# Kernel optimization log

Measured on AMD Instinct MI355X. Metric: run time of the kernel, lower is better.

Reference implementation:

```python
import jax, jax.numpy as jnp
import numpy as np

D_MODEL = 1024
N_HEADS = 16
D_HEAD = D_MODEL // N_HEADS


def setup_inputs() -> dict:
    key = jax.random.key(0)
    ks = jax.random.split(key, 7)
    x = jax.random.normal(ks[0], (1, 4096, D_MODEL), dtype=jnp.float32)
    # torch Linear default init ~ U(-1/sqrt(fan_in), 1/sqrt(fan_in)); small randn is fine for a reference
    Wqkv = jax.random.normal(ks[1], (3 * D_MODEL, D_MODEL), dtype=jnp.float32) * (1.0 / np.sqrt(D_MODEL))
    bqkv = jax.random.normal(ks[2], (3 * D_MODEL,), dtype=jnp.float32) * 0.01
    Wo = jax.random.normal(ks[3], (D_MODEL, D_MODEL), dtype=jnp.float32) * (1.0 / np.sqrt(D_MODEL))
    bo = jax.random.normal(ks[4], (D_MODEL,), dtype=jnp.float32) * 0.01
    wq = jnp.ones((D_HEAD,), dtype=jnp.float32)
    wk = jnp.ones((D_HEAD,), dtype=jnp.float32)
    return {"x": x, "Wqkv": Wqkv, "bqkv": bqkv, "Wo": Wo, "bo": bo, "wq": wq, "wk": wk}


def _rmsnorm(x, w):
    # matches RMSNormRef: mean of squares over last dim, eps added to mean before sqrt
    xf = x.astype(jnp.float32)
    rms = jnp.mean(xf * xf, axis=-1, keepdims=True)
    return (xf / jnp.sqrt(rms + 1e-6) * w.astype(jnp.float32)).astype(x.dtype)


def reference(x, Wqkv, bqkv, Wo, bo, wq, wk):
    b, s, d = x.shape
    qkv = x @ Wqkv.T + bqkv                       # [b, s, 3d]
    q, k, v = jnp.split(qkv, 3, axis=-1)
    q = q.reshape(b, s, N_HEADS, D_HEAD)
    k = k.reshape(b, s, N_HEADS, D_HEAD)
    v = v.reshape(b, s, N_HEADS, D_HEAD)
    q = _rmsnorm(q, wq)
    k = _rmsnorm(k, wk)
    # NOTE: original applies NO 1/sqrt(d_head) scaling and NO causal mask
    qf = q.astype(jnp.float32)
    kf = k.astype(jnp.float32)
    vf = v.astype(jnp.float32)
    attn = jnp.einsum('bqhd,bkhd->bhqk', qf, kf)  # [b, h, s, s] fp32 scores
    attn = jax.nn.softmax(attn, axis=-1)
    z = jnp.einsum('bhqk,bkhd->bqhd', attn, vf).astype(x.dtype)
    z = z.reshape(b, s, d)
    return z @ Wo.T + bo
```

## Files before the change

### kernel.cpp

```cpp
#include <hip/hip_runtime.h>
#include <hip/hip_bf16.h>

typedef __bf16 bf16;
typedef bf16 bf16x8 __attribute__((ext_vector_type(8)));
typedef bf16 bf16x4 __attribute__((ext_vector_type(4)));
typedef float f32x4 __attribute__((ext_vector_type(4)));

static constexpr int SEQ    = 4096;
static constexpr int DMODEL = 1024;
static constexpr int NHEADS = 16;
static constexpr int DHEAD  = 64;
static constexpr int QKV3   = 3 * DMODEL;
static constexpr float SMAX = 64.0f;

__device__ inline void gld16(const bf16* g, bf16* l) {
    __builtin_amdgcn_global_load_lds(
        (const __attribute__((address_space(1))) void*)g,
        (__attribute__((address_space(3))) void*)l, 16, 0, 0);
}

__device__ inline bf16x8 load8(const float* src) {
    float4 a = *(const float4*)(src);
    float4 b = *(const float4*)(src + 4);
    bf16x8 r;
    r[0] = (bf16)a.x; r[1] = (bf16)a.y; r[2] = (bf16)a.z; r[3] = (bf16)a.w;
    r[4] = (bf16)b.x; r[5] = (bf16)b.y; r[6] = (bf16)b.z; r[7] = (bf16)b.w;
    return r;
}

static constexpr size_t NX = (size_t)SEQ * DMODEL;
static constexpr size_t NW = (size_t)QKV3 * DMODEL;
static constexpr size_t NO = (size_t)DMODEL * DMODEL;

__global__ __launch_bounds__(256)
void cvt_all(const float* __restrict__ x, const float* __restrict__ Wqkv,
             const float* __restrict__ Wo, bf16* __restrict__ outbase) {
    const size_t e = ((size_t)blockIdx.x * 256 + threadIdx.x) * 8;
    const float* src;
    if (e < NX)            src = x + e;
    else if (e < NX + NW)  src = Wqkv + (e - NX);
    else                   src = Wo + (e - NX - NW);
    *(bf16x8*)(outbase + e) = load8(src);
}

__global__ __launch_bounds__(256)
void gemm_qkv(const bf16* __restrict__ A, const bf16* __restrict__ W,
              const float* __restrict__ bias, const float* __restrict__ wq,
              const float* __restrict__ wk, bf16* __restrict__ qkv,
              bf16* __restrict__ Vt) {
    __shared__ __align__(16) bf16 As[128 * 32];
    __shared__ __align__(16) bf16 Ws[128 * 32];
    const int tid  = threadIdx.x;
    const int wave = tid >> 6;
    const int ll   = tid & 15;
    const int quad = (tid & 63) >> 4;
    const int wm   = (wave >> 1) * 64;
    const int wn   = (wave & 1) * 64;
    const int m0 = blockIdx.y * 128;
    const int n0 = blockIdx.x * 128;

    f32x4 acc[4][4];
#pragma unroll
    for (int i = 0; i < 4; ++i)
#pragma unroll
        for (int j = 0; j < 4; ++j) acc[i][j] = (f32x4){0.f, 0.f, 0.f, 0.f};

    for (int k0 = 0; k0 < DMODEL; k0 += 32) {
        __syncthreads();
#pragma unroll
        for (int i = 0; i < 2; ++i) {
            const int idx = i * 256 + tid;
            const int row = idx >> 2;
            const int c   = (idx & 3) ^ ((row >> 1) & 3);
            gld16(&A[(size_t)(m0 + row) * DMODEL + k0 + c * 8], As + idx * 8);
            gld16(&W[(size_t)(n0 + row) * DMODEL + k0 + c * 8], Ws + idx * 8);
        }
        __syncthreads();
        bf16x8 af[4], bfr[4];
#pragma unroll
        for (int mi = 0; mi < 4; ++mi) {
            const int row = wm + mi * 16 + ll;
            af[mi] = *(const bf16x8*)(As + (row * 4 + (quad ^ ((ll >> 1) & 3))) * 8);
        }
#pragma unroll
        for (int ni = 0; ni < 4; ++ni) {
            const int row = wn + ni * 16 + ll;
            bfr[ni] = *(const bf16x8*)(Ws + (row * 4 + (quad ^ ((ll >> 1) & 3))) * 8);
        }
#pragma unroll
        for (int mi = 0; mi < 4; ++mi)
#pragma unroll
            for (int ni = 0; ni < 4; ++ni)
                acc[mi][ni] = __builtin_amdgcn_mfma_f32_16x16x32_bf16(
                    af[mi], bfr[ni], acc[mi][ni], 0, 0, 0);
    }

    float bvn[4];
#pragma unroll
    for (int ni = 0; ni < 4; ++ni) bvn[ni] = bias[n0 + wn + ni * 16 + ll];

    const int sect = (n0 + wn) >> 10;
    if (sect < 2) {
        const float* wv = sect ? wk : wq;
        float wvl[4];
#pragma unroll
        for (int ni = 0; ni < 4; ++ni) wvl[ni] = wv[ni * 16 + ll];
#pragma unroll
        for (int mi = 0; mi < 4; ++mi)
#pragma unroll
            for (int r = 0; r < 4; ++r) {
                float xf[4];
                float ss = 0.f;
#pragma unroll
                for (int ni = 0; ni < 4; ++ni) {
                    xf[ni] = (float)(bf16)(acc[mi][ni][r] + bvn[ni]);
                    ss += xf[ni] * xf[ni];
                }
#pragma unroll
                for (int off = 1; off < 16; off <<= 1) ss += __shfl_xor(ss, off);
                const float scale = rsqrtf(ss * (1.0f / 64.0f) + 1e-6f);
                const int row = m0 + wm + mi * 16 + quad * 4 + r;
#pragma unroll
                for (int ni = 0; ni < 4; ++ni)
                    qkv[(size_t)row * QKV3 + n0 + wn + ni * 16 + ll] =
                        (bf16)(xf[ni] * scale * wvl[ni]);
            }
    } else {
        const int h = (n0 + wn - 2 * DMODEL) >> 6;
#pragma unroll
        for (int mi = 0; mi < 4; ++mi) {
            const int kv = m0 + wm + mi * 16 + quad * 4;
#pragma unroll
            for (int ni = 0; ni < 4; ++ni) {
                bf16x4 vv;
#pragma unroll
                for (int r = 0; r < 4; ++r) vv[r] = (bf16)(acc[mi][ni][r] + bvn[ni]);
                *(bf16x4*)(Vt + (size_t)(h * DHEAD + ni * 16 + ll) * SEQ + kv) = vv;
            }
        }
    }
}

__global__ __launch_bounds__(256)
void gemm_out(const bf16* __restrict__ A, const bf16* __restrict__ W,
              const float* __restrict__ bias, float* __restrict__ C) {
    __shared__ __align__(16) bf16 As[128 * 32];
    __shared__ __align__(16) bf16 Ws[64 * 32];
    const int tid  = threadIdx.x;
    const int wave = tid >> 6;
    const int ll   = tid & 15;
    const int quad = (tid & 63) >> 4;
    const int m0 = blockIdx.y * 128;
    const int n0 = blockIdx.x * 64;

    f32x4 acc[2][4];
#pragma unroll
    for (int i = 0; i < 2; ++i)
#pragma unroll
        for (int j = 0; j < 4; ++j) acc[i][j] = (f32x4){0.f, 0.f, 0.f, 0.f};

    for (int k0 = 0; k0 < DMODEL; k0 += 32) {
        __syncthreads();
#pragma unroll
        for (int i = 0; i < 2; ++i) {
            const int idx = i * 256 + tid;
            const int row = idx >> 2;
            const int c   = (idx & 3) ^ ((row >> 1) & 3);
            gld16(&A[(size_t)(m0 + row) * DMODEL + k0 + c * 8], As + idx * 8);
        }
        {
            const int j   = tid;
            const int row = j >> 2;
            const int c   = (j & 3) ^ ((row >> 1) & 3);
            gld16(&W[(size_t)(n0 + row) * DMODEL + k0 + c * 8], Ws + j * 8);
        }
        __syncthreads();
        bf16x8 af[2], bfr[4];
#pragma unroll
        for (int mi = 0; mi < 2; ++mi) {
            const int row = wave * 32 + mi * 16 + ll;
            af[mi] = *(const bf16x8*)(As + (row * 4 + (quad ^ ((ll >> 1) & 3))) * 8);
        }
#pragma unroll
        for (int ni = 0; ni < 4; ++ni) {
            const int row = ni * 16 + ll;
            bfr[ni] = *(const bf16x8*)(Ws + (row * 4 + (quad ^ ((ll >> 1) & 3))) * 8);
        }
#pragma unroll
        for (int mi = 0; mi < 2; ++mi)
#pragma unroll
            for (int ni = 0; ni < 4; ++ni)
                acc[mi][ni] = __builtin_amdgcn_mfma_f32_16x16x32_bf16(
                    af[mi], bfr[ni], acc[mi][ni], 0, 0, 0);
    }
#pragma unroll
    for (int ni = 0; ni < 4; ++ni) {
        const int col = n0 + ni * 16 + ll;
        const float bv = bias[col];
#pragma unroll
        for (int mi = 0; mi < 2; ++mi)
#pragma unroll
            for (int r = 0; r < 4; ++r) {
                const int row = m0 + wave * 32 + mi * 16 + quad * 4 + r;
                C[(size_t)row * DMODEL + col] = acc[mi][ni][r] + bv;
            }
    }
}

template<bool PARTIAL>
__global__ __launch_bounds__(256, 4)
void attn_fwd(const bf16* __restrict__ qkv, const bf16* __restrict__ Vt,
              bf16* __restrict__ z, float* __restrict__ opf,
              float* __restrict__ lsum) {
    __shared__ __align__(16) bf16 Ks[64 * 64];
    __shared__ __align__(16) bf16 VTs[64 * 64];
    __shared__ __align__(16) bf16 Ps[128 * 72];

    const int tid  = threadIdx.x;
    const int wave = tid >> 6;
    const int ll   = tid & 15;
    const int quad = (tid & 63) >> 4;
    const int head = blockIdx.x;
    const int q0   = blockIdx.y * 128;
    const int half = PARTIAL ? blockIdx.z : 0;
    const int kvbeg = half * (SEQ / 2);
    const int kvlen = PARTIAL ? (SEQ / 2) : SEQ;
    const int wrow = wave * 32;

    const bf16* kbase  = qkv + DMODEL + head * DHEAD;
    const bf16* vtbase = Vt + (size_t)head * DHEAD * SEQ;

#pragma unroll
    for (int i = 0; i < 4; ++i) {
        const int idx = i * 256 + tid;
        const int row = idx >> 3;
        const int c   = (idx & 7) ^ (row & 7);
        gld16(qkv + (size_t)(q0 + row) * QKV3 + head * DHEAD + c * 8, Ps + idx * 8);
    }
    __syncthreads();
    bf16x8 aq[2][2];
#pragma unroll
    for (int sub = 0; sub < 2; ++sub)
#pragma unroll
        for (int ks = 0; ks < 2; ++ks) {
            const int row = wrow + sub * 16 + ll;
            const int pc  = (ks * 4 + quad) ^ (ll & 7);
            aq[sub][ks] = *(const bf16x8*)(Ps + (row * 8 + pc) * 8);
        }

    f32x4 lp[2];
    f32x4 o[2][4];
#pragma unroll
    for (int sub = 0; sub < 2; ++sub) {
        lp[sub] = (f32x4){0.f, 0.f, 0.f, 0.f};
#pragma unroll
        for (int nt = 0; nt < 4; ++nt) o[sub][nt] = (f32x4){0.f, 0.f, 0.f, 0.f};
    }

    for (int kv0 = kvbeg; kv0 < kvbeg + kvlen; kv0 += 64) {
        __syncthreads();
#pragma unroll
        for (int i = 0; i < 2; ++i) {
            const int idx = i * 256 + tid;
            const int row = idx >> 3;
            const int c   = (idx & 7) ^ (row & 7);
            gld16(kbase + (size_t)(kv0 + row) * QKV3 + c * 8, Ks + idx * 8);
            gld16(vtbase + (size_t)row * SEQ + kv0 + c * 8, VTs + idx * 8);
        }
        __syncthreads();

        f32x4 s[2][4];
#pragma unroll
        for (int nt = 0; nt < 4; ++nt) {
            s[0][nt] = (f32x4){0.f, 0.f, 0.f, 0.f};
            s[1][nt] = (f32x4){0.f, 0.f, 0.f, 0.f};
        }
#pragma unroll
        for (int ks = 0; ks < 2; ++ks)
#pragma unroll
            for (int nt = 0; nt < 4; ++nt) {
                const int row = nt * 16 + ll;
                const int pc  = (ks * 4 + quad) ^ (ll & 7);
                bf16x8 b = *(const bf16x8*)(Ks + (row * 8 + pc) * 8);
                s[0][nt] = __builtin_amdgcn_mfma_f32_16x16x32_bf16(aq[0][ks], b, s[0][nt], 0, 0, 0);
                s[1][nt] = __builtin_amdgcn_mfma_f32_16x16x32_bf16(aq[1][ks], b, s[1][nt], 0, 0, 0);
            }

#pragma unroll
        for (int sub = 0; sub < 2; ++sub) {
#pragma unroll
            for (int nt = 0; nt < 4; ++nt)
#pragma unroll
                for (int r = 0; r < 4; ++r) {
                    const float p2 = __expf(s[sub][nt][r] - SMAX);
                    s[sub][nt][r] = p2;
                    lp[sub][r] += p2;
                }
#pragma unroll
            for (int nt = 0; nt < 4; ++nt)
#pragma unroll
                for (int r = 0; r < 4; ++r)
                    Ps[(wrow + sub * 16 + quad * 4 + r) * 72 + nt * 16 + ll] =
                        (bf16)s[sub][nt][r];
        }

#pragma unroll
        for (int ks = 0; ks < 2; ++ks) {
            bf16x8 a0 = *(const bf16x8*)(Ps + (wrow + ll) * 72 + ks * 32 + quad * 8);
            bf16x8 a1 = *(const bf16x8*)(Ps + (wrow + 16 + ll) * 72 + ks * 32 + quad * 8);
#pragma unroll
            for (int nt = 0; nt < 4; ++nt) {
                const int row = nt * 16 + ll;
                const int pc  = (ks * 4 + quad) ^ (ll & 7);
                bf16x8 b = *(const bf16x8*)(VTs + (row * 8 + pc) * 8);
                o[0][nt] = __builtin_amdgcn_mfma_f32_16x16x32_bf16(a0, b, o[0][nt], 0, 0, 0);
                o[1][nt] = __builtin_amdgcn_mfma_f32_16x16x32_bf16(a1, b, o[1][nt], 0, 0, 0);
            }
        }
    }

#pragma unroll
    for (int sub = 0; sub < 2; ++sub) {
#pragma unroll
        for (int off = 1; off < 16; off <<= 1)
#pragma unroll
            for (int r = 0; r < 4; ++r) lp[sub][r] += __shfl_xor(lp[sub][r], off);

        if (PARTIAL) {
#pragma unroll
            for (int nt = 0; nt < 4; ++nt) {
                const int col = head * DHEAD + nt * 16 + ll;
#pragma unroll
                for (int r = 0; r < 4; ++r) {
                    const int row = q0 + wrow + sub * 16 + quad * 4 + r;
                    opf[((size_t)half * SEQ + row) * DMODEL + col] = o[sub][nt][r];
                }
            }
            if (ll == 0) {
#pragma unroll
                for (int r = 0; r < 4; ++r) {
                    const int row = q0 + wrow + sub * 16 + quad * 4 + r;
                    lsum[((size_t)half * SEQ + row) * NHEADS + head] = lp[sub][r];
                }
            }
        } else {
#pragma unroll
            for (int nt = 0; nt < 4; ++nt) {
                const int d = head * DHEAD + nt * 16 + ll;
#pragma unroll
                for (int r = 0; r < 4; ++r) {
                    const int row = q0 + wrow + sub * 16 + quad * 4 + r;
                    z[(size_t)row * DMODEL + d] = (bf16)(o[sub][nt][r] / lp[sub][r]);
                }
            }
        }
    }
}

__global__ __launch_bounds__(256)
void combine_halves(const float* __restrict__ opf, const float* __restrict__ lsum,
                    bf16* __restrict__ z) {
    const int row = blockIdx.x;
    const int c   = threadIdx.x * 4;
    const int head = c >> 6;
    const float l = lsum[(size_t)row * NHEADS + head] +
                    lsum[((size_t)SEQ + row) * NHEADS + head];
    const float4 o0 = *(const float4*)(opf + (size_t)row * DMODEL + c);
    const float4 o1 = *(const float4*)(opf + ((size_t)SEQ + row) * DMODEL + c);
    bf16x4 out;
    out[0] = (bf16)((o0.x + o1.x) / l);
    out[1] = (bf16)((o0.y + o1.y) / l);
    out[2] = (bf16)((o0.z + o1.z) / l);
    out[3] = (bf16)((o0.w + o1.w) / l);
    *(bf16x4*)(z + (size_t)row * DMODEL + c) = out;
}

extern "C" void kernel_launch(void* const* d_in, const int* in_sizes, int n_in,
                              void* d_out, int out_size, void* d_ws, size_t ws_size,
                              hipStream_t stream) {
    const float* x    = (const float*)d_in[0];
    const float* Wqkv = (const float*)d_in[1];
    const float* bqkv = (const float*)d_in[2];
    const float* Wo   = (const float*)d_in[3];
    const float* bo   = (const float*)d_in[4];
    const float* wq   = (const float*)d_in[5];
    const float* wk   = (const float*)d_in[6];
    float* out = (float*)d_out;

    bf16* qkv  = (bf16*)d_ws;
    bf16* z    = qkv + (size_t)SEQ * QKV3;
    bf16* Vt   = z + (size_t)SEQ * DMODEL;
    bf16* xb   = Vt + (size_t)NHEADS * DHEAD * SEQ;
    bf16* Wqb  = xb + NX;
    bf16* Wob  = Wqb + NW;
    bf16* endb = Wob + NO;
    float* opf  = (float*)endb;
    float* lsum = opf + (size_t)2 * SEQ * DMODEL;
    const size_t need = (size_t)((char*)(lsum + (size_t)2 * SEQ * NHEADS) - (char*)d_ws);
    const bool split = ws_size >= need;

    cvt_all<<<dim3((NX + NW + NO) / 2048), 256, 0, stream>>>(x, Wqkv, Wo, xb);

    gemm_qkv<<<dim3(QKV3 / 128, SEQ / 128), 256, 0, stream>>>(
        xb, Wqb, bqkv, wq, wk, qkv, Vt);

    if (split) {
        attn_fwd<true><<<dim3(NHEADS, SEQ / 128, 2), 256, 0, stream>>>(
            qkv, Vt, z, opf, lsum);
        combine_halves<<<dim3(SEQ), 256, 0, stream>>>(opf, lsum, z);
    } else {
        attn_fwd<false><<<dim3(NHEADS, SEQ / 128, 1), 256, 0, stream>>>(
            qkv, Vt, z, nullptr, nullptr);
    }

    gemm_out<<<dim3(DMODEL / 64, SEQ / 128), 256, 0, stream>>>(z, Wob, bo, out);
}
```

Baseline: 260.1 us.

## Rewrite attention inner loop with 32x32 MFMA computing transposed scores in registers

Switches the attention kernel from 16x16x32 to 32x32x16 bf16 MFMAs and computes S^T = K·Q^T so that each lane's score outputs can be packed with v_cvt_pk_bf16_f32 and rearranged via v_permlane32_swap into the B-operand layout for the PV MFMA. This removes the round trip of P through shared memory and the associated LDS writes and reads each KV tile. The epilogue now stages outputs through a per-wave LDS buffer to produce vectorized global stores. It depends on a precise register-layout mapping through inline asm, and the larger accumulators may increase register pressure.

Measured after the change: 241.4 us. 7.2% less time.

```diff
diff --git a/kernel.cpp b/kernel.cpp
--- a/kernel.cpp
+++ b/kernel.cpp
@@ -5,6 +5,9 @@
 typedef bf16 bf16x8 __attribute__((ext_vector_type(8)));
 typedef bf16 bf16x4 __attribute__((ext_vector_type(4)));
 typedef float f32x4 __attribute__((ext_vector_type(4)));
+typedef float f32x16 __attribute__((ext_vector_type(16)));
+typedef unsigned int u32;
+typedef u32 u32x4 __attribute__((ext_vector_type(4)));
 
 static constexpr int SEQ    = 4096;
 static constexpr int DMODEL = 1024;
@@ -25,6 +28,13 @@
     bf16x8 r;
     r[0] = (bf16)a.x; r[1] = (bf16)a.y; r[2] = (bf16)a.z; r[3] = (bf16)a.w;
     r[4] = (bf16)b.x; r[5] = (bf16)b.y; r[6] = (bf16)b.z; r[7] = (bf16)b.w;
+    return r;
+}
+
+__device__ inline f32x16 zero16() {
+    f32x16 r;
+#pragma unroll
+    for (int i = 0; i < 16; ++i) r[i] = 0.f;
     return r;
 }
 
@@ -214,48 +224,41 @@
               float* __restrict__ lsum) {
     __shared__ __align__(16) bf16 Ks[64 * 64];
     __shared__ __align__(16) bf16 VTs[64 * 64];
-    __shared__ __align__(16) bf16 Ps[128 * 72];
+    __shared__ __align__(16) float Os[4][32][36];
 
     const int tid  = threadIdx.x;
     const int wave = tid >> 6;
-    const int ll   = tid & 15;
-    const int quad = (tid & 63) >> 4;
+    const int lane = tid & 63;
+    const int l31  = lane & 31;
+    const int hh   = lane >> 5;
+    const int l7   = lane & 7;
     const int head = blockIdx.x;
     const int q0   = blockIdx.y * 128;
     const int half = PARTIAL ? blockIdx.z : 0;
     const int kvbeg = half * (SEQ / 2);
     const int kvlen = PARTIAL ? (SEQ / 2) : SEQ;
-    const int wrow = wave * 32;
 
     const bf16* kbase  = qkv + DMODEL + head * DHEAD;
     const bf16* vtbase = Vt + (size_t)head * DHEAD * SEQ;
 
+    bf16* Qs = (bf16*)&Os[0][0][0];
 #pragma unroll
     for (int i = 0; i < 4; ++i) {
         const int idx = i * 256 + tid;
         const int row = idx >> 3;
         const int c   = (idx & 7) ^ (row & 7);
-        gld16(qkv + (size_t)(q0 + row) * QKV3 + head * DHEAD + c * 8, Ps + idx * 8);
+        gld16(qkv + (size_t)(q0 + row) * QKV3 + head * DHEAD + c * 8, Qs + idx * 8);
     }
     __syncthreads();
-    bf16x8 aq[2][2];
-#pragma unroll
-    for (int sub = 0; sub < 2; ++sub)
-#pragma unroll
-        for (int ks = 0; ks < 2; ++ks) {
-            const int row = wrow + sub * 16 + ll;
-            const int pc  = (ks * 4 + quad) ^ (ll & 7);
-            aq[sub][ks] = *(const bf16x8*)(Ps + (row * 8 + pc) * 8);
-        }
-
-    f32x4 lp[2];
-    f32x4 o[2][4];
-#pragma unroll
-    for (int sub = 0; sub < 2; ++sub) {
-        lp[sub] = (f32x4){0.f, 0.f, 0.f, 0.f};
-#pragma unroll
-        for (int nt = 0; nt < 4; ++nt) o[sub][nt] = (f32x4){0.f, 0.f, 0.f, 0.f};
-    }
+    bf16x8 qf[4];
+#pragma unroll
+    for (int kd = 0; kd < 4; ++kd)
+        qf[kd] = *(const bf16x8*)(Qs + ((wave * 32 + l31) * 8 + ((kd * 2 + hh) ^ l7)) * 8);
+
+    f32x16 o[2];
+    o[0] = zero16();
+    o[1] = zero16();
+    float lp = 0.f;
 
     for (int kv0 = kvbeg; kv0 < kvbeg + kvlen; kv0 += 64) {
         __syncthreads();
@@ -269,89 +272,72 @@
         }
         __syncthreads();
 
-        f32x4 s[2][4];
-#pragma unroll
-        for (int nt = 0; nt < 4; ++nt) {
-            s[0][nt] = (f32x4){0.f, 0.f, 0.f, 0.f};
-            s[1][nt] = (f32x4){0.f, 0.f, 0.f, 0.f};
-        }
-#pragma unroll
-        for (int ks = 0; ks < 2; ++ks)
-#pragma unroll
-            for (int nt = 0; nt < 4; ++nt) {
-                const int row = nt * 16 + ll;
-                const int pc  = (ks * 4 + quad) ^ (ll & 7);
-                bf16x8 b = *(const bf16x8*)(Ks + (row * 8 + pc) * 8);
-                s[0][nt] = __builtin_amdgcn_mfma_f32_16x16x32_bf16(aq[0][ks], b, s[0][nt], 0, 0, 0);
-                s[1][nt] = __builtin_amdgcn_mfma_f32_16x16x32_bf16(aq[1][ks], b, s[1][nt], 0, 0, 0);
-            }
-
-#pragma unroll
-        for (int sub = 0; sub < 2; ++sub) {
-#pragma unroll
-            for (int nt = 0; nt < 4; ++nt)
-#pragma unroll
-                for (int r = 0; r < 4; ++r) {
-                    const float p2 = __expf(s[sub][nt][r] - SMAX);
-                    s[sub][nt][r] = p2;
-                    lp[sub][r] += p2;
+#pragma unroll
+        for (int kvt = 0; kvt < 2; ++kvt) {
+            f32x16 st = zero16();
+#pragma unroll
+            for (int kd = 0; kd < 4; ++kd) {
+                bf16x8 kf = *(const bf16x8*)(
+                    Ks + ((kvt * 32 + l31) * 8 + ((kd * 2 + hh) ^ l7)) * 8);
+                st = __builtin_amdgcn_mfma_f32_32x32x16_bf16(kf, qf[kd], st, 0, 0, 0);
+            }
+            float pf[16];
+#pragma unroll
+            for (int r = 0; r < 16; ++r) {
+                pf[r] = __expf(st[r] - SMAX);
+                lp += pf[r];
+            }
+#pragma unroll
+            for (int cc = 0; cc < 2; ++cc) {
+                u32 a1, b1, a2, b2;
+                asm("v_cvt_pk_bf16_f32 %0, %1, %2" : "=v"(a1) : "v"(pf[8 * cc + 0]), "v"(pf[8 * cc + 1]));
+                asm("v_cvt_pk_bf16_f32 %0, %1, %2" : "=v"(b1) : "v"(pf[8 * cc + 4]), "v"(pf[8 * cc + 5]));
+                asm("v_cvt_pk_bf16_f32 %0, %1, %2" : "=v"(a2) : "v"(pf[8 * cc + 2]), "v"(pf[8 * cc + 3]));
+                asm("v_cvt_pk_bf16_f32 %0, %1, %2" : "=v"(b2) : "v"(pf[8 * cc + 6]), "v"(pf[8 * cc + 7]));
+                asm("v_permlane32_swap_b32 %0, %1" : "+v"(a1), "+v"(b1));
+                asm("v_permlane32_swap_b32 %0, %1" : "+v"(a2), "+v"(b2));
+                u32x4 w;
+                w[0] = a1; w[1] = a2; w[2] = b1; w[3] = b2;
+                const bf16x8 bp = *(const bf16x8*)&w;
+                const int c = kvt * 2 + cc;
+#pragma unroll
+                for (int dt = 0; dt < 2; ++dt) {
+                    bf16x8 vf = *(const bf16x8*)(
+                        VTs + ((dt * 32 + l31) * 8 + ((c * 2 + hh) ^ l7)) * 8);
+                    o[dt] = __builtin_amdgcn_mfma_f32_32x32x16_bf16(vf, bp, o[dt], 0, 0, 0);
                 }
-#pragma unroll
-            for (int nt = 0; nt < 4; ++nt)
-#pragma unroll
-                for (int r = 0; r < 4; ++r)
-                    Ps[(wrow + sub * 16 + quad * 4 + r) * 72 + nt * 16 + ll] =
-                        (bf16)s[sub][nt][r];
-        }
-
-#pragma unroll
-        for (int ks = 0; ks < 2; ++ks) {
-            bf16x8 a0 = *(const bf16x8*)(Ps + (wrow + ll) * 72 + ks * 32 + quad * 8);
-            bf16x8 a1 = *(const bf16x8*)(Ps + (wrow + 16 + ll) * 72 + ks * 32 + quad * 8);
-#pragma unroll
-            for (int nt = 0; nt < 4; ++nt) {
-                const int row = nt * 16 + ll;
-                const int pc  = (ks * 4 + quad) ^ (ll & 7);
-                bf16x8 b = *(const bf16x8*)(VTs + (row * 8 + pc) * 8);
-                o[0][nt] = __builtin_amdgcn_mfma_f32_16x16x32_bf16(a0, b, o[0][nt], 0, 0, 0);
-                o[1][nt] = __builtin_amdgcn_mfma_f32_16x16x32_bf16(a1, b, o[1][nt], 0, 0, 0);
-            }
-        }
-    }
-
-#pragma unroll
-    for (int sub = 0; sub < 2; ++sub) {
-#pragma unroll
-        for (int off = 1; off < 16; off <<= 1)
-#pragma unroll
-            for (int r = 0; r < 4; ++r) lp[sub][r] += __shfl_xor(lp[sub][r], off);
-
-        if (PARTIAL) {
-#pragma unroll
-            for (int nt = 0; nt < 4; ++nt) {
-                const int col = head * DHEAD + nt * 16 + ll;
-#pragma unroll
-                for (int r = 0; r < 4; ++r) {
-                    const int row = q0 + wrow + sub * 16 + quad * 4 + r;
-                    opf[((size_t)half * SEQ + row) * DMODEL + col] = o[sub][nt][r];
-                }
-            }
-            if (ll == 0) {
-#pragma unroll
-                for (int r = 0; r < 4; ++r) {
-                    const int row = q0 + wrow + sub * 16 + quad * 4 + r;
-                    lsum[((size_t)half * SEQ + row) * NHEADS + head] = lp[sub][r];
-                }
-            }
-        } else {
-#pragma unroll
-            for (int nt = 0; nt < 4; ++nt) {
-                const int d = head * DHEAD + nt * 16 + ll;
-#pragma unroll
-                for (int r = 0; r < 4; ++r) {
-                    const int row = q0 + wrow + sub * 16 + quad * 4 + r;
-                    z[(size_t)row * DMODEL + d] = (bf16)(o[sub][nt][r] / lp[sub][r]);
-                }
+            }
+        }
+    }
+
+    lp += __shfl_xor(lp, 32);
+    const int qrow = q0 + wave * 32 + l31;
+    if (PARTIAL) {
+        if (lane < 32) lsum[((size_t)half * SEQ + qrow) * NHEADS + head] = lp;
+    }
+    const float inv = PARTIAL ? 1.0f : 1.0f / lp;
+
+#pragma unroll
+    for (int dt = 0; dt < 2; ++dt) {
+#pragma unroll
+        for (int r = 0; r < 16; ++r) {
+            const int dl = (r & 3) + 8 * (r >> 2) + 4 * hh;
+            Os[wave][l31][dl] = o[dt][r] * inv;
+        }
+#pragma unroll
+        for (int it = 0; it < 4; ++it) {
+            const int qr  = it * 8 + (lane >> 3);
+            const int dl2 = (lane & 7) * 4;
+            const f32x4 v = *(const f32x4*)(&Os[wave][qr][dl2]);
+            const int row = q0 + wave * 32 + qr;
+            const int col = head * DHEAD + dt * 32 + dl2;
+            if (PARTIAL) {
+                *(f32x4*)(opf + ((size_t)half * SEQ + row) * DMODEL + col) = v;
+            } else {
+                bf16x4 ov;
+                ov[0] = (bf16)v[0]; ov[1] = (bf16)v[1];
+                ov[2] = (bf16)v[2]; ov[3] = (bf16)v[3];
+                *(bf16x4*)(z + (size_t)row * DMODEL + col) = ov;
             }
         }
     }
```
